# Optimization experiments

Hardware: AMD Instinct MI355X
Metric: run time of the kernel (lower is better)

The kernel has to match this reference:

```python
import jax, jax.numpy as jnp
import numpy as np

B, LQ, LK, H = 16, 8192, 128, 128  # note LK == H is required by the final matmul
SCALE = float(np.sqrt(H))


def setup_inputs() -> dict:
    key = jax.random.key(0)
    k1, k2, k3, k4, k5, k6 = jax.random.split(key, 6)
    x1 = jax.random.normal(k1, (B, LQ, H), dtype=jnp.float32)
    x2 = jax.random.normal(k2, (B, LK, H), dtype=jnp.float32)
    x3 = jax.random.randint(k3, (B, LQ, LK), 0, 2).astype(bool)
    bound = 1.0 / np.sqrt(H)  # torch Linear default init
    wq = jax.random.uniform(k4, (H, H), minval=-bound, maxval=bound, dtype=jnp.float32)
    wk = jax.random.uniform(k5, (H, H), minval=-bound, maxval=bound, dtype=jnp.float32)
    wv = jax.random.uniform(k6, (H, H), minval=-bound, maxval=bound, dtype=jnp.float32)
    return {"x1": x1, "x2": x2, "x3": x3, "wq": wq, "wk": wk, "wv": wv}


def reference(x1, x2, x3, wq, wk, wv):
    q = x1 @ wq.T                                   # (B, Lq, H)
    k = x2 @ wk.T                                   # (B, Lk, H)
    qk = jnp.einsum('bqh,bkh->bqk', q, k) / SCALE   # (B, Lq, Lk)
    qk = jnp.where(x3, -jnp.inf, qk)                # masked_fill_ where mask is True
    attn_weight = jax.nn.softmax(qk, axis=-1)       # softmax over Lk
    v = x2 @ wv.T                                   # (B, Lk, H)
    # v @ attn_weight^T: contracts v's H axis with attn_weight's Lk axis (H == Lk)
    attn = jnp.matmul(v, jnp.swapaxes(attn_weight, -2, -1))  # (B, Lk, Lq)
    return attn
```

## Files before the change

kernel.cpp:

```cpp
#include <hip/hip_runtime.h>
#include <hip/hip_bf16.h>
#include <stdint.h>

typedef __bf16 bf16_t;
typedef __bf16 bf16x8 __attribute__((ext_vector_type(8)));
typedef float  f32x4  __attribute__((ext_vector_type(4)));
typedef float  f32x16 __attribute__((ext_vector_type(16)));
typedef unsigned int uint;
typedef uint uintx4 __attribute__((ext_vector_type(4)));

#define MFMA16(a,b,c) __builtin_amdgcn_mfma_f32_16x16x32_bf16((a),(b),(c),0,0,0)
#define MFMA32(a,b,c) __builtin_amdgcn_mfma_f32_32x32x16_bf16((a),(b),(c),0,0,0)

constexpr int NB = 16;
constexpr int LQ = 8192;
constexpr int LK = 128;
constexpr int H  = 128;

constexpr float C1 = 1.4426950408889634f / 11.313708498984761f;

constexpr size_t WS_FLAG = 0;
constexpr size_t WS_MV   = 1024;

__device__ __forceinline__ unsigned swz(unsigned row, unsigned byte) {
  return row * 256u + (byte ^ ((row & 15u) << 4));
}

__device__ __forceinline__ bf16x8 cvt_frag(const float* p) {
  f32x4 u0 = *(const f32x4*)p;
  f32x4 u1 = *(const f32x4*)(p + 4);
  bf16x8 v;
  #pragma unroll
  for (int e = 0; e < 4; ++e) { v[e] = (bf16_t)u0[e]; v[e + 4] = (bf16_t)u1[e]; }
  return v;
}

__device__ __forceinline__ f32x16 zero16() {
  f32x16 z;
  #pragma unroll
  for (int i = 0; i < 16; ++i) z[i] = 0.f;
  return z;
}

__device__ __forceinline__ uint pkbf(float a, float b) {
  uint d;
  asm("v_cvt_pk_bf16_f32 %0, %1, %2" : "=v"(d) : "v"(a), "v"(b));
  return d;
}

__device__ __forceinline__ void gl16(const void* g, void* l) {
  __builtin_amdgcn_global_load_lds(
      (const __attribute__((address_space(1))) uint32_t*)g,
      (__attribute__((address_space(3))) uint32_t*)l, 16, 0, 0);
}

__global__ __launch_bounds__(512) void prep_kernel(
    const float* __restrict__ x2, const float* __restrict__ wq,
    const float* __restrict__ wk, const float* __restrict__ wv,
    const unsigned* __restrict__ x3w, uint8_t* __restrict__ ws)
{
  __shared__ uint8_t sP[131072];
  __shared__ int sF32, sBig;
  const int tid = threadIdx.x;
  const int b = blockIdx.x >> 1, which = blockIdx.x & 1;
  const int l = tid & 63, w = tid >> 6, q31 = l & 31, hi2 = l >> 5;
  uint8_t* sOut = sP + 98304;

  if (which == 0) {
    if (blockIdx.x == 0) {
      if (tid == 0) { sF32 = 0; sBig = 0; }
      __syncthreads();
      int f = 0, g = 0;
      #pragma unroll
      for (int j = 0; j < 4; ++j) {
        unsigned v = x3w[tid * 4 + j];
        if (v == 0x3f800000u) f = 1;
        else if (v > 1u) g = 1;
      }
      if (f) sF32 = 1;
      if (g) sBig = 1;
      __syncthreads();
      if (tid == 0) *(int*)(ws + WS_FLAG) = (sF32 == 0 && sBig == 1) ? 1 : 0;
    }

    {
      const int row = tid >> 2, c0 = (tid & 3) * 32;
      #pragma unroll
      for (int wh = 0; wh < 2; ++wh) {
        const float* W = wh ? wk : wq;
        uint8_t* dst = sP + wh * 32768;
        const float* s = W + row * H + c0;
        #pragma unroll
        for (int j = 0; j < 32; ++j)
          *(bf16_t*)(dst + swz(c0 + j, row * 2)) = (bf16_t)s[j];
      }
    }
    __syncthreads();

    {
      const int lo = l & 15, hi = l >> 4;
      bf16x8 a4[4];
      #pragma unroll
      for (int kk = 0; kk < 4; ++kk)
        a4[kk] = *(const bf16x8*)(sP + swz(16 * w + lo, kk * 64 + hi * 16));
      bf16_t* W2T = (bf16_t*)(sP + 65536);
      #pragma unroll
      for (int t = 0; t < 8; ++t) {
        f32x4 c = {0.f, 0.f, 0.f, 0.f};
        #pragma unroll
        for (int kk = 0; kk < 4; ++kk)
          c = MFMA16(a4[kk], *(const bf16x8*)(sP + 32768 + swz(16 * t + lo, kk * 64 + hi * 16)), c);
        #pragma unroll
        for (int r = 0; r < 4; ++r)
          W2T[(16 * w + hi * 4 + r) * H + 16 * t + lo] = (bf16_t)c[r];
      }
    }
    __syncthreads();

    if (w < 4) {
      const int wb = w;
      bf16x8 axf[8];
      const float* x2r = x2 + ((size_t)b * LK + 32 * wb + q31) * H;
      #pragma unroll
      for (int kt = 0; kt < 8; ++kt)
        axf[kt] = cvt_frag(x2r + kt * 16 + 8 * hi2);
      const bf16_t* W2Tl = (const bf16_t*)(sP + 65536);
      #pragma unroll
      for (int nt = 0; nt < 4; ++nt) {
        f32x16 c = zero16();
        #pragma unroll
        for (int kt = 0; kt < 8; ++kt)
          c = MFMA32(axf[kt],
                     *(const bf16x8*)(W2Tl + (size_t)(nt * 32 + q31) * H + kt * 16 + 8 * hi2), c);
        #pragma unroll
        for (int r = 0; r < 16; ++r)
          *(bf16_t*)(sOut + swz(32 * wb + (r & 3) + 8 * (r >> 2) + 4 * hi2,
                                (nt * 32 + q31) * 2)) = (bf16_t)c[r];
      }
    }
  } else {
    if (w < 4) {
      const int wb = w;
      bf16x8 axf[8];
      const float* x2r = x2 + ((size_t)b * LK + 32 * wb + q31) * H;
      #pragma unroll
      for (int kt = 0; kt < 8; ++kt)
        axf[kt] = cvt_frag(x2r + kt * 16 + 8 * hi2);
      #pragma unroll
      for (int nt = 0; nt < 4; ++nt) {
        f32x16 c = zero16();
        #pragma unroll
        for (int kt = 0; kt < 8; ++kt)
          c = MFMA32(axf[kt],
                     cvt_frag(wv + (size_t)(nt * 32 + q31) * H + kt * 16 + 8 * hi2), c);
        #pragma unroll
        for (int r = 0; r < 16; ++r)
          *(bf16_t*)(sOut + swz(32 * wb + (r & 3) + 8 * (r >> 2) + 4 * hi2,
                                (nt * 32 + q31) * 2)) = (bf16_t)c[r];
      }
    }
  }
  __syncthreads();

  {
    const uint4* src = (const uint4*)sOut;
    uint4* dst = (uint4*)(ws + WS_MV + (size_t)b * 65536 + (size_t)which * 32768);
    #pragma unroll
    for (int j = 0; j < 4; ++j)
      dst[tid + j * 512] = src[tid + j * 512];
  }
}

__global__ __launch_bounds__(512, 4) void attn_kernel(
    const float* __restrict__ x1, const void* __restrict__ x3,
    const uint8_t* __restrict__ ws, float* __restrict__ out)
{
  __shared__ uint8_t sm[65536];
  uint8_t* sM = sm;
  uint8_t* sV = sm + 32768;

  const int tid = threadIdx.x, blk = blockIdx.x;
  const int b = blk >> 5, qc = (blk & 31) * 256;
  const int l = tid & 63, w = tid >> 6;
  const int q31 = l & 31, hi2 = l >> 5;
  const int byteMode = *(const int*)(ws + WS_FLAG);

  const int q0w = qc + w * 32;
  const size_t qrow = (size_t)b * LQ + q0w + q31;

  {
    const uint8_t* g = ws + WS_MV + (size_t)b * 65536;
    #pragma unroll
    for (int j = 0; j < 8; ++j)
      gl16(g + tid * 16 + j * 8192, sm + tid * 16 + j * 8192);
  }

  f32x4 xr[16];
  {
    const float* xp = x1 + qrow * H;
    #pragma unroll
    for (int kt = 0; kt < 8; ++kt) {
      xr[2 * kt]     = *(const f32x4*)(xp + kt * 16 + 8 * hi2);
      xr[2 * kt + 1] = *(const f32x4*)(xp + kt * 16 + 8 * hi2 + 4);
    }
  }

  uint mu[16];
  if (byteMode) {
    const uint8_t* mp = (const uint8_t*)x3 + qrow * LK;
    #pragma unroll
    for (int jt = 0; jt < 4; ++jt)
      #pragma unroll
      for (int rg = 0; rg < 4; ++rg)
        mu[jt * 4 + rg] = *(const uint*)(mp + jt * 32 + 8 * rg + 4 * hi2);
  }
  __syncthreads();

  bf16x8 xbf[8];
  #pragma unroll
  for (int kt = 0; kt < 8; ++kt)
    #pragma unroll
    for (int e = 0; e < 4; ++e) {
      xbf[kt][e]     = (bf16_t)xr[2 * kt][e];
      xbf[kt][e + 4] = (bf16_t)xr[2 * kt + 1][e];
    }

  const uint* mrowW = (const uint*)x3 + qrow * LK;
  bf16x8 pb[8];

  #pragma unroll
  for (int half = 0; half < 2; ++half) {
    const int jt0 = half * 2, jt1 = half * 2 + 1;
    f32x16 s0 = zero16(), s1 = zero16();
    __builtin_amdgcn_s_setprio(1);
    #pragma unroll
    for (int kt = 0; kt < 8; ++kt) {
      s0 = MFMA32(*(const bf16x8*)(sM + swz(jt0 * 32 + q31, kt * 32 + hi2 * 16)),
                  xbf[kt], s0);
      s1 = MFMA32(*(const bf16x8*)(sM + swz(jt1 * 32 + q31, kt * 32 + hi2 * 16)),
                  xbf[kt], s1);
    }
    __builtin_amdgcn_s_setprio(0);

    #pragma unroll
    for (int jj = 0; jj < 2; ++jj) {
      f32x16& sj = jj ? s1 : s0;
      const int jt = half * 2 + jj;
      #pragma unroll
      for (int rg = 0; rg < 4; ++rg) {
        uint m0, m1, m2, m3;
        if (byteMode) {
          uint u = mu[jt * 4 + rg];
          m0 = u & 0xffu; m1 = (u >> 8) & 0xffu; m2 = (u >> 16) & 0xffu; m3 = u >> 24;
        } else {
          uint4 mw = *(const uint4*)(mrowW + jt * 32 + 8 * rg + 4 * hi2);
          m0 = mw.x; m1 = mw.y; m2 = mw.z; m3 = mw.w;
        }
        float p0 = __builtin_amdgcn_exp2f(sj[rg * 4 + 0] * C1);
        float p1 = __builtin_amdgcn_exp2f(sj[rg * 4 + 1] * C1);
        float p2 = __builtin_amdgcn_exp2f(sj[rg * 4 + 2] * C1);
        float p3 = __builtin_amdgcn_exp2f(sj[rg * 4 + 3] * C1);
        sj[rg * 4 + 0] = m0 ? 0.f : p0;
        sj[rg * 4 + 1] = m1 ? 0.f : p1;
        sj[rg * 4 + 2] = m2 ? 0.f : p2;
        sj[rg * 4 + 3] = m3 ? 0.f : p3;
      }

      #pragma unroll
      for (int h = 0; h < 2; ++h) {
        uint A = pkbf(sj[h * 8 + 0], sj[h * 8 + 1]);
        uint C = pkbf(sj[h * 8 + 2], sj[h * 8 + 3]);
        uint B = pkbf(sj[h * 8 + 4], sj[h * 8 + 5]);
        uint D = pkbf(sj[h * 8 + 6], sj[h * 8 + 7]);
        asm("v_permlane32_swap_b32 %0, %1" : "+v"(A), "+v"(B));
        asm("v_permlane32_swap_b32 %0, %1" : "+v"(C), "+v"(D));
        uintx4 t; t.x = A; t.y = C; t.z = B; t.w = D;
        pb[jt * 2 + h] = __builtin_bit_cast(bf16x8, t);
      }
    }
  }

  bf16x8 ones1;
  #pragma unroll
  for (int e = 0; e < 8; ++e) ones1[e] = (bf16_t)1.f;

  f32x16 dacc = zero16();
  {
    f32x16 o0 = zero16(), o1 = zero16();
    __builtin_amdgcn_s_setprio(1);
    #pragma unroll
    for (int kt = 0; kt < 8; ++kt) {
      dacc = MFMA32(ones1, pb[kt], dacc);
      o0 = MFMA32(*(const bf16x8*)(sV + swz(0 * 32 + q31, kt * 32 + hi2 * 16)), pb[kt], o0);
      o1 = MFMA32(*(const bf16x8*)(sV + swz(1 * 32 + q31, kt * 32 + hi2 * 16)), pb[kt], o1);
    }
    __builtin_amdgcn_s_setprio(0);
    const float inv = 1.0f / dacc[0];
    #pragma unroll
    for (int r = 0; r < 16; ++r) {
      const int ibase = (r & 3) + 8 * (r >> 2) + 4 * hi2;
      out[((size_t)b * LK + ibase) * LQ + q0w + q31] = o0[r] * inv;
      out[((size_t)b * LK + 32 + ibase) * LQ + q0w + q31] = o1[r] * inv;
    }
  }

  {
    const float inv = 1.0f / dacc[0];
    f32x16 o2 = zero16(), o3 = zero16();
    __builtin_amdgcn_s_setprio(1);
    #pragma unroll
    for (int kt = 0; kt < 8; ++kt) {
      o2 = MFMA32(*(const bf16x8*)(sV + swz(2 * 32 + q31, kt * 32 + hi2 * 16)), pb[kt], o2);
      o3 = MFMA32(*(const bf16x8*)(sV + swz(3 * 32 + q31, kt * 32 + hi2 * 16)), pb[kt], o3);
    }
    __builtin_amdgcn_s_setprio(0);
    #pragma unroll
    for (int r = 0; r < 16; ++r) {
      const int ibase = (r & 3) + 8 * (r >> 2) + 4 * hi2;
      out[((size_t)b * LK + 64 + ibase) * LQ + q0w + q31] = o2[r] * inv;
      out[((size_t)b * LK + 96 + ibase) * LQ + q0w + q31] = o3[r] * inv;
    }
  }
}

extern "C" void kernel_launch(void* const* d_in, const int* in_sizes, int n_in,
                              void* d_out, int out_size, void* d_ws, size_t ws_size,
                              hipStream_t stream) {
  const float* x1 = (const float*)d_in[0];
  const float* x2 = (const float*)d_in[1];
  const void*  x3 = d_in[2];
  const float* wq = (const float*)d_in[3];
  const float* wk = (const float*)d_in[4];
  const float* wv = (const float*)d_in[5];
  uint8_t* ws = (uint8_t*)d_ws;
  float* out = (float*)d_out;

  prep_kernel<<<2 * NB, 512, 0, stream>>>(x2, wq, wk, wv, (const unsigned*)x3, ws);
  attn_kernel<<<NB * (LQ / 256), 512, 0, stream>>>(x1, x3, ws, out);
}
```

Measured before the change: 49.50 us.

## Pre-pack M/V into MFMA fragment order and read directly from global, dropping LDS

The prep kernel now writes the M and V operands in per-lane MFMA fragment order, so the attention kernel can load each fragment straight from global memory (through cache) as one contiguous 16-byte load per lane. The LDS staging, the global_load_lds path and the block barrier go away, and the attention kernel switches to 256-thread blocks covering 128 queries with twice as many blocks. This trades LDS traffic and the sync for repeated global/L2 reads of the 64KB per-batch operand block by every wave, which adds latency inside the MFMA loops.

```diff
diff --git a/kernel.cpp b/kernel.cpp
--- a/kernel.cpp
+++ b/kernel.cpp
@@ -46,12 +46,6 @@
   uint d;
   asm("v_cvt_pk_bf16_f32 %0, %1, %2" : "=v"(d) : "v"(a), "v"(b));
   return d;
-}
-
-__device__ __forceinline__ void gl16(const void* g, void* l) {
-  __builtin_amdgcn_global_load_lds(
-      (const __attribute__((address_space(1))) uint32_t*)g,
-      (__attribute__((address_space(3))) uint32_t*)l, 16, 0, 0);
 }
 
 __global__ __launch_bounds__(512) void prep_kernel(
@@ -163,37 +157,34 @@
   __syncthreads();
 
   {
-    const uint4* src = (const uint4*)sOut;
-    uint4* dst = (uint4*)(ws + WS_MV + (size_t)b * 65536 + (size_t)which * 32768);
-    #pragma unroll
-    for (int j = 0; j < 4; ++j)
-      dst[tid + j * 512] = src[tid + j * 512];
-  }
-}
-
-__global__ __launch_bounds__(512, 4) void attn_kernel(
+    uint8_t* dst = ws + WS_MV + (size_t)b * 65536 + (size_t)which * 32768;
+    #pragma unroll
+    for (int pass = 0; pass < 4; ++pass) {
+      const int idx = tid + pass * 512;
+      const int chunk = idx >> 6, le = idx & 63;
+      const int t4 = chunk >> 3, kt = chunk & 7;
+      bf16x8 v = *(const bf16x8*)(sOut + swz(t4 * 32 + (le & 31),
+                                             kt * 32 + (le >> 5) * 16));
+      *(bf16x8*)(dst + (size_t)idx * 16) = v;
+    }
+  }
+}
+
+__global__ __launch_bounds__(256, 4) void attn_kernel(
     const float* __restrict__ x1, const void* __restrict__ x3,
     const uint8_t* __restrict__ ws, float* __restrict__ out)
 {
-  __shared__ uint8_t sm[65536];
-  uint8_t* sM = sm;
-  uint8_t* sV = sm + 32768;
-
   const int tid = threadIdx.x, blk = blockIdx.x;
-  const int b = blk >> 5, qc = (blk & 31) * 256;
-  const int l = tid & 63, w = tid >> 6;
+  const int b = blk >> 6, qc = (blk & 63) * 128;
+  const int l = tid & 63, w4 = tid >> 6;
   const int q31 = l & 31, hi2 = l >> 5;
   const int byteMode = *(const int*)(ws + WS_FLAG);
 
-  const int q0w = qc + w * 32;
+  const int q0w = qc + w4 * 32;
   const size_t qrow = (size_t)b * LQ + q0w + q31;
 
-  {
-    const uint8_t* g = ws + WS_MV + (size_t)b * 65536;
-    #pragma unroll
-    for (int j = 0; j < 8; ++j)
-      gl16(g + tid * 16 + j * 8192, sm + tid * 16 + j * 8192);
-  }
+  const uint8_t* Mf = ws + WS_MV + (size_t)b * 65536;
+  const uint8_t* Vf = Mf + 32768;
 
   f32x4 xr[16];
   {
@@ -214,7 +205,6 @@
       for (int rg = 0; rg < 4; ++rg)
         mu[jt * 4 + rg] = *(const uint*)(mp + jt * 32 + 8 * rg + 4 * hi2);
   }
-  __syncthreads();
 
   bf16x8 xbf[8];
   #pragma unroll
@@ -235,9 +225,9 @@
     __builtin_amdgcn_s_setprio(1);
     #pragma unroll
     for (int kt = 0; kt < 8; ++kt) {
-      s0 = MFMA32(*(const bf16x8*)(sM + swz(jt0 * 32 + q31, kt * 32 + hi2 * 16)),
+      s0 = MFMA32(*(const bf16x8*)(Mf + (((jt0 * 8 + kt) << 10) | (l << 4))),
                   xbf[kt], s0);
-      s1 = MFMA32(*(const bf16x8*)(sM + swz(jt1 * 32 + q31, kt * 32 + hi2 * 16)),
+      s1 = MFMA32(*(const bf16x8*)(Mf + (((jt1 * 8 + kt) << 10) | (l << 4))),
                   xbf[kt], s1);
     }
     __builtin_amdgcn_s_setprio(0);
@@ -291,8 +281,8 @@
     #pragma unroll
     for (int kt = 0; kt < 8; ++kt) {
       dacc = MFMA32(ones1, pb[kt], dacc);
-      o0 = MFMA32(*(const bf16x8*)(sV + swz(0 * 32 + q31, kt * 32 + hi2 * 16)), pb[kt], o0);
-      o1 = MFMA32(*(const bf16x8*)(sV + swz(1 * 32 + q31, kt * 32 + hi2 * 16)), pb[kt], o1);
+      o0 = MFMA32(*(const bf16x8*)(Vf + (((0 * 8 + kt) << 10) | (l << 4))), pb[kt], o0);
+      o1 = MFMA32(*(const bf16x8*)(Vf + (((1 * 8 + kt) << 10) | (l << 4))), pb[kt], o1);
     }
     __builtin_amdgcn_s_setprio(0);
     const float inv = 1.0f / dacc[0];
@@ -305,15 +295,15 @@
   }
 
   {
-    const float inv = 1.0f / dacc[0];
     f32x16 o2 = zero16(), o3 = zero16();
     __builtin_amdgcn_s_setprio(1);
     #pragma unroll
     for (int kt = 0; kt < 8; ++kt) {
-      o2 = MFMA32(*(const bf16x8*)(sV + swz(2 * 32 + q31, kt * 32 + hi2 * 16)), pb[kt], o2);
-      o3 = MFMA32(*(const bf16x8*)(sV + swz(3 * 32 + q31, kt * 32 + hi2 * 16)), pb[kt], o3);
+      o2 = MFMA32(*(const bf16x8*)(Vf + (((2 * 8 + kt) << 10) | (l << 4))), pb[kt], o2);
+      o3 = MFMA32(*(const bf16x8*)(Vf + (((3 * 8 + kt) << 10) | (l << 4))), pb[kt], o3);
     }
     __builtin_amdgcn_s_setprio(0);
+    const float inv = 1.0f / dacc[0];
     #pragma unroll
     for (int r = 0; r < 16; ++r) {
       const int ibase = (r & 3) + 8 * (r >> 2) + 4 * hi2;
@@ -336,5 +326,5 @@
   float* out = (float*)d_out;
 
   prep_kernel<<<2 * NB, 512, 0, stream>>>(x2, wq, wk, wv, (const unsigned*)x3, ws);
-  attn_kernel<<<NB * (LQ / 256), 512, 0, stream>>>(x1, x3, ws, out);
-}
+  attn_kernel<<<NB * (LQ / 128), 256, 0, stream>>>(x1, x3, ws, out);
+}
```

After: 51.15 us. 3.3% more time.
